# Kernel optimization log

Hardware: AMD Instinct MI355X
Metric: run time of the kernel (lower is better)

The kernel has to match this reference:

```python
import math
import jax, jax.numpy as jnp
import numpy as np

INP_MODES = [4, 8, 8, 4]   # prod = 1024 = in_features
OUT_MODES = [8, 8, 8, 8]   # prod = 4096 = out_features
TT_RANKS = [1, 8, 8, 8, 1]
IN_FEATURES = 1024
OUT_FEATURES = 4096
BATCH = 8192
D = len(INP_MODES)


def setup_inputs() -> dict:
    key = jax.random.key(0)
    ks = jax.random.split(key, D + 2)
    inp = {"x": jax.random.normal(ks[0], (BATCH, IN_FEATURES), dtype=jnp.float32)}
    for i in range(D):
        # xavier_normal per the module's reset_parameters
        fan_in = TT_RANKS[i] * INP_MODES[i]
        fan_out = TT_RANKS[i + 1] * OUT_MODES[i]
        std = math.sqrt(2.0 / (fan_in + fan_out))
        shape = (TT_RANKS[i] * OUT_MODES[i], TT_RANKS[i + 1] * INP_MODES[i])
        inp[f"core{i}"] = std * jax.random.normal(ks[i + 1], shape, dtype=jnp.float32)
    bound = 1.0 / math.sqrt(IN_FEATURES)
    inp["bias"] = jax.random.uniform(ks[D + 1], (OUT_FEATURES,), dtype=jnp.float32,
                                     minval=-bound, maxval=bound)
    return inp


def _tt_forward(x, cores, bias):
    # x: [B, in_features]. Sequentially contract input modes against TT cores.
    # Invariant after step i: h has shape (B, M=prod(m_0..m_i), r_{i+1}, N=prod(n_{i+1}..))
    B = x.shape[0]
    h = x.reshape(B, 1, 1, IN_FEATURES)
    for i, c in enumerate(cores):
        r, m, q, n = TT_RANKS[i], OUT_MODES[i], TT_RANKS[i + 1], INP_MODES[i]
        c4 = c.reshape(r, m, q, n)          # (r_i, m_i, r_{i+1}, n_i)
        M = h.shape[1]
        h = h.reshape(B, M, r, n, -1)       # split current input mode n_i
        # contract rank r_i and input mode n_i; produce out mode m_i (s) and next rank q
        h = jnp.einsum('bmrnp,rsqn->bmsqp', h, c4)
        h = h.reshape(B, M * m, q, -1)
    y = h.reshape(B, OUT_FEATURES) + bias
    return y


def reference(x, core0, core1, core2, core3, bias):
    return _tt_forward(x, [core0, core1, core2, core3], bias)
```

## Files before the change

### kernel.cpp

```cpp
#include <hip/hip_runtime.h>
#include <hip/hip_bf16.h>

typedef __bf16 bf16x4 __attribute__((ext_vector_type(4)));
typedef __bf16 bf16x8 __attribute__((ext_vector_type(8)));
typedef float  f32x4  __attribute__((ext_vector_type(4)));
typedef float  f32x16 __attribute__((ext_vector_type(16)));

#define MFMA32(a,b,c) __builtin_amdgcn_mfma_f32_32x32x16_bf16((a),(b),(c),0,0,0)


__global__ __launch_bounds__(256) void tt_kernel(
    const float* __restrict__ x,  const float* __restrict__ c0,
    const float* __restrict__ c1, const float* __restrict__ c2,
    const float* __restrict__ c3, const float* __restrict__ bias,
    float* __restrict__ y)
{
    __shared__ __align__(16) __bf16 w23l[16384];
    __shared__ __align__(16) __bf16 xt[2048];
    __shared__ __align__(16) __bf16 hb[16384];

    const int tid  = threadIdx.x;
    const int wid  = tid >> 6;
    const int lane = tid & 63;
    const int hh   = lane >> 5;
    const int c32  = lane & 31;
    const int rt   = wid & 1;
    const int ct   = wid >> 1;

    {
      const int r = tid >> 2, kb = (tid & 3) * 64;
      const int m2 = r >> 3, m3 = r & 7;
      float c3v[8][4];
      #pragma unroll
      for (int r3 = 0; r3 < 8; ++r3)
        #pragma unroll
        for (int n3 = 0; n3 < 4; ++n3)
          c3v[r3][n3] = c3[(r3 * 8 + m3) * 4 + n3];
      for (int j = 0; j < 64; ++j) {
        const int k = kb + j;
        const int n2 = k >> 5, n3 = (k >> 3) & 3, r2 = k & 7;
        float s = 0.f;
        #pragma unroll
        for (int r3 = 0; r3 < 8; ++r3)
          s += c2[(r2 * 8 + m2) * 64 + r3 * 8 + n2] * c3v[r3][n3];
        w23l[r * 256 + (((k >> 3) ^ (r & 31)) << 3) + (k & 7)] = (__bf16)s;
      }
    }

    bf16x8 w01f[8][2];
    {
      const int row = rt * 32 + c32, m1 = row >> 3, r2w = row & 7;
      float c1row[8][8];
      #pragma unroll
      for (int r1 = 0; r1 < 8; ++r1)
        #pragma unroll
        for (int n1 = 0; n1 < 8; ++n1)
          c1row[r1][n1] = c1[(r1 * 8 + m1) * 64 + r2w * 8 + n1];
      for (int m0 = 0; m0 < 8; ++m0) {
        #pragma unroll
        for (int kt = 0; kt < 2; ++kt) {
          const int n0 = kt * 2 + hh;
          #pragma unroll
          for (int j = 0; j < 8; ++j) {
            float s = 0.f;
            #pragma unroll
            for (int r1 = 0; r1 < 8; ++r1)
              s += c0[m0 * 32 + r1 * 4 + n0] * c1row[r1][j];
            w01f[m0][kt][j] = (__bf16)s;
          }
        }
      }
    }

    for (int it = 0; it < 8; ++it) {
      const int b0 = (blockIdx.x * 8 + it) * 2;

      {
        const int bsel = tid >> 7, col = tid & 31, k0q = (tid >> 5) & 3;
        const float* xp = x + (size_t)(b0 + bsel) * 1024 + col;
        bf16x8 v;
        #pragma unroll
        for (int j = 0; j < 8; ++j) v[j] = (__bf16)xp[(k0q * 8 + j) * 32];
        *(bf16x8*)&xt[(bsel * 32 + col) * 32 + ((k0q ^ (col & 3)) << 3)] = v;
      }
      __syncthreads();

      bf16x8 xf[2];
      #pragma unroll
      for (int kt = 0; kt < 2; ++kt)
        xf[kt] = *(const bf16x8*)
          &xt[(ct * 32 + c32) * 32 + (((kt * 2 + hh) ^ (c32 & 3)) << 3)];

      #pragma unroll
      for (int q = 0; q < 2; ++q) {
        #pragma unroll
        for (int m0h = 0; m0h < 4; ++m0h) {
          f32x16 acc = {};
          acc = MFMA32(w01f[q * 4 + m0h][0], xf[0], acc);
          acc = MFMA32(w01f[q * 4 + m0h][1], xf[1], acc);
          #pragma unroll
          for (int p = 0; p < 4; ++p) {
            bf16x4 o;
            #pragma unroll
            for (int i = 0; i < 4; ++i) o[i] = (__bf16)acc[p * 4 + i];
            const int cl = ct * 32 + m0h * 8 + rt * 4 + p;
            *(bf16x4*)&hb[cl * 256 + ((c32 ^ (cl & 31)) << 3) + hh * 4] = o;
          }
        }
        __syncthreads();

        const __bf16* arow = &w23l[(rt * 32 + c32) * 256];
        const __bf16* brow = &hb[(ct * 32 + c32) * 256];
        f32x16 acc2 = {};
        #pragma unroll
        for (int kt = 0; kt < 16; ++kt) {
          const int op = ((kt * 2 + hh) ^ c32) << 3;
          const bf16x8 af = *(const bf16x8*)&arow[op];
          const bf16x8 bf = *(const bf16x8*)&brow[op];
          acc2 = MFMA32(af, bf, acc2);
        }

        const size_t ybase = (size_t)(b0 + ct) * 4096;
        const int boff = (q * 4 + (c32 >> 3)) * 512 + (c32 & 7) * 64 + hh * 4;
        #pragma unroll
        for (int p = 0; p < 4; ++p) {
          const int off = boff + (rt * 4 + p) * 8;
          const f32x4 bv = *(const f32x4*)&bias[off];
          f32x4 o;
          #pragma unroll
          for (int i = 0; i < 4; ++i) o[i] = acc2[p * 4 + i] + bv[i];
          *(f32x4*)&y[ybase + off] = o;
        }
        __syncthreads();
      }
    }
}

extern "C" void kernel_launch(void* const* d_in, const int* in_sizes, int n_in,
                              void* d_out, int out_size, void* d_ws, size_t ws_size,
                              hipStream_t stream) {
    const float* x    = (const float*)d_in[0];
    const float* c0   = (const float*)d_in[1];
    const float* c1   = (const float*)d_in[2];
    const float* c2   = (const float*)d_in[3];
    const float* c3   = (const float*)d_in[4];
    const float* bias = (const float*)d_in[5];
    float* yout = (float*)d_out;
    tt_kernel<<<512, 256, 0, stream>>>(x, c0, c1, c2, c3, bias, yout);
}
```

Before: 229.5 us.

## Keep W23 fragments in registers, double-buffer x tiles, and reduce block barriers

Loads the W23 MFMA fragments into registers once per block, which removes their LDS reads from the inner loop. Reuses the W23 LDS region as a second h buffer. The batch loop is restructured into two explicit halves, and the next x tile is prefetched into a double-buffered LDS slot while the current one is consumed, so each iteration needs fewer barriers. It also adds nontemporal output stores and a launch-bounds occupancy hint of 2. The cost is higher VGPR pressure, which could cause spills or lower occupancy.

```diff
diff --git a/kernel.cpp b/kernel.cpp
--- a/kernel.cpp
+++ b/kernel.cpp
@@ -9,15 +9,17 @@
 #define MFMA32(a,b,c) __builtin_amdgcn_mfma_f32_32x32x16_bf16((a),(b),(c),0,0,0)
 
 
-__global__ __launch_bounds__(256) void tt_kernel(
+__global__ __launch_bounds__(256, 2) void tt_kernel(
     const float* __restrict__ x,  const float* __restrict__ c0,
     const float* __restrict__ c1, const float* __restrict__ c2,
     const float* __restrict__ c3, const float* __restrict__ bias,
     float* __restrict__ y)
 {
-    __shared__ __align__(16) __bf16 w23l[16384];
-    __shared__ __align__(16) __bf16 xt[2048];
-    __shared__ __align__(16) __bf16 hb[16384];
+    __shared__ __align__(16) __bf16 smem[36864];
+    __bf16* w23l = smem;
+    __bf16* hb1  = smem;
+    __bf16* hb0  = smem + 16384;
+    __bf16* xtb  = smem + 32768;
 
     const int tid  = threadIdx.x;
     const int wid  = tid >> 6;
@@ -71,57 +73,61 @@
         }
       }
     }
+    __syncthreads();
+
+    bf16x8 w23f[16];
+    {
+      const __bf16* arow = &w23l[(rt * 32 + c32) * 256];
+      #pragma unroll
+      for (int kt = 0; kt < 16; ++kt)
+        w23f[kt] = *(const bf16x8*)&arow[(((kt * 2 + hh) ^ c32) << 3)];
+    }
+
+    {
+      const int bsel = tid >> 7, col = tid & 31, k0q = (tid >> 5) & 3;
+      const float* xp = x + (size_t)(blockIdx.x * 16 + bsel) * 1024 + col;
+      bf16x8 v;
+      #pragma unroll
+      for (int j = 0; j < 8; ++j) v[j] = (__bf16)xp[(k0q * 8 + j) * 32];
+      *(bf16x8*)&xtb[(bsel * 32 + col) * 32 + ((k0q ^ (col & 3)) << 3)] = v;
+    }
+    __syncthreads();
+
+    bf16x8 xf[2];
+    #pragma unroll
+    for (int kt = 0; kt < 2; ++kt)
+      xf[kt] = *(const bf16x8*)
+        &xtb[(ct * 32 + c32) * 32 + (((kt * 2 + hh) ^ (c32 & 3)) << 3)];
 
     for (int it = 0; it < 8; ++it) {
       const int b0 = (blockIdx.x * 8 + it) * 2;
 
+      #pragma unroll
+      for (int m0h = 0; m0h < 4; ++m0h) {
+        f32x16 acc = {};
+        acc = MFMA32(w01f[m0h][0], xf[0], acc);
+        acc = MFMA32(w01f[m0h][1], xf[1], acc);
+        #pragma unroll
+        for (int p = 0; p < 4; ++p) {
+          bf16x4 o;
+          #pragma unroll
+          for (int i = 0; i < 4; ++i) o[i] = (__bf16)acc[p * 4 + i];
+          const int cl = ct * 32 + m0h * 8 + rt * 4 + p;
+          *(bf16x4*)&hb0[cl * 256 + ((c32 ^ (cl & 31)) << 3) + hh * 4] = o;
+        }
+      }
+      __syncthreads();
+
       {
-        const int bsel = tid >> 7, col = tid & 31, k0q = (tid >> 5) & 3;
-        const float* xp = x + (size_t)(b0 + bsel) * 1024 + col;
-        bf16x8 v;
-        #pragma unroll
-        for (int j = 0; j < 8; ++j) v[j] = (__bf16)xp[(k0q * 8 + j) * 32];
-        *(bf16x8*)&xt[(bsel * 32 + col) * 32 + ((k0q ^ (col & 3)) << 3)] = v;
-      }
-      __syncthreads();
-
-      bf16x8 xf[2];
-      #pragma unroll
-      for (int kt = 0; kt < 2; ++kt)
-        xf[kt] = *(const bf16x8*)
-          &xt[(ct * 32 + c32) * 32 + (((kt * 2 + hh) ^ (c32 & 3)) << 3)];
-
-      #pragma unroll
-      for (int q = 0; q < 2; ++q) {
-        #pragma unroll
-        for (int m0h = 0; m0h < 4; ++m0h) {
-          f32x16 acc = {};
-          acc = MFMA32(w01f[q * 4 + m0h][0], xf[0], acc);
-          acc = MFMA32(w01f[q * 4 + m0h][1], xf[1], acc);
-          #pragma unroll
-          for (int p = 0; p < 4; ++p) {
-            bf16x4 o;
-            #pragma unroll
-            for (int i = 0; i < 4; ++i) o[i] = (__bf16)acc[p * 4 + i];
-            const int cl = ct * 32 + m0h * 8 + rt * 4 + p;
-            *(bf16x4*)&hb[cl * 256 + ((c32 ^ (cl & 31)) << 3) + hh * 4] = o;
-          }
-        }
-        __syncthreads();
-
-        const __bf16* arow = &w23l[(rt * 32 + c32) * 256];
-        const __bf16* brow = &hb[(ct * 32 + c32) * 256];
+        const __bf16* brow = &hb0[(ct * 32 + c32) * 256];
         f32x16 acc2 = {};
         #pragma unroll
-        for (int kt = 0; kt < 16; ++kt) {
-          const int op = ((kt * 2 + hh) ^ c32) << 3;
-          const bf16x8 af = *(const bf16x8*)&arow[op];
-          const bf16x8 bf = *(const bf16x8*)&brow[op];
-          acc2 = MFMA32(af, bf, acc2);
-        }
-
+        for (int kt = 0; kt < 16; ++kt)
+          acc2 = MFMA32(w23f[kt],
+                        *(const bf16x8*)&brow[(((kt * 2 + hh) ^ c32) << 3)],
+                        acc2);
         const size_t ybase = (size_t)(b0 + ct) * 4096;
-        const int boff = (q * 4 + (c32 >> 3)) * 512 + (c32 & 7) * 64 + hh * 4;
+        const int boff = (c32 >> 3) * 512 + (c32 & 7) * 64 + hh * 4;
         #pragma unroll
         for (int p = 0; p < 4; ++p) {
           const int off = boff + (rt * 4 + p) * 8;
@@ -129,9 +135,61 @@
           f32x4 o;
           #pragma unroll
           for (int i = 0; i < 4; ++i) o[i] = acc2[p * 4 + i] + bv[i];
-          *(f32x4*)&y[ybase + off] = o;
-        }
-        __syncthreads();
+          __builtin_nontemporal_store(o, (f32x4*)&y[ybase + off]);
+        }
+      }
+
+      #pragma unroll
+      for (int m0h = 0; m0h < 4; ++m0h) {
+        f32x16 acc = {};
+        acc = MFMA32(w01f[4 + m0h][0], xf[0], acc);
+        acc = MFMA32(w01f[4 + m0h][1], xf[1], acc);
+        #pragma unroll
+        for (int p = 0; p < 4; ++p) {
+          bf16x4 o;
+          #pragma unroll
+          for (int i = 0; i < 4; ++i) o[i] = (__bf16)acc[p * 4 + i];
+          const int cl = ct * 32 + m0h * 8 + rt * 4 + p;
+          *(bf16x4*)&hb1[cl * 256 + ((c32 ^ (cl & 31)) << 3) + hh * 4] = o;
+        }
+      }
+      if (it < 7) {
+        const int bsel = tid >> 7, col = tid & 31, k0q = (tid >> 5) & 3;
+        const float* xp = x + (size_t)(b0 + 2 + bsel) * 1024 + col;
+        bf16x8 v;
+        #pragma unroll
+        for (int j = 0; j < 8; ++j) v[j] = (__bf16)xp[(k0q * 8 + j) * 32];
+        *(bf16x8*)&xtb[((it + 1) & 1) * 2048 + (bsel * 32 + col) * 32 +
+                       ((k0q ^ (col & 3)) << 3)] = v;
+      }
+      __syncthreads();
+
+      {
+        const __bf16* brow = &hb1[(ct * 32 + c32) * 256];
+        f32x16 acc2 = {};
+        #pragma unroll
+        for (int kt = 0; kt < 16; ++kt)
+          acc2 = MFMA32(w23f[kt],
+                        *(const bf16x8*)&brow[(((kt * 2 + hh) ^ c32) << 3)],
+                        acc2);
+        const size_t ybase = (size_t)(b0 + ct) * 4096;
+        const int boff = (4 + (c32 >> 3)) * 512 + (c32 & 7) * 64 + hh * 4;
+        #pragma unroll
+        for (int p = 0; p < 4; ++p) {
+          const int off = boff + (rt * 4 + p) * 8;
+          const f32x4 bv = *(const f32x4*)&bias[off];
+          f32x4 o;
+          #pragma unroll
+          for (int i = 0; i < 4; ++i) o[i] = acc2[p * 4 + i] + bv[i];
+          __builtin_nontemporal_store(o, (f32x4*)&y[ybase + off]);
+        }
+      }
+      if (it < 7) {
+        const __bf16* xq = &xtb[((it + 1) & 1) * 2048];
+        #pragma unroll
+        for (int kt = 0; kt < 2; ++kt)
+          xf[kt] = *(const bf16x8*)
+            &xq[(ct * 32 + c32) * 32 + (((kt * 2 + hh) ^ (c32 & 3)) << 3)];
       }
     }
 }
```

Result: slower. 298.4 us (+30.0%).
